# Kernel tuning notes

Measured on AMD Instinct MI355X. Metric: run time of the kernel, lower is better.

The kernel has to match this reference:

```python
import jax, jax.numpy as jnp
import numpy as np
import math

HEAD_DIM = 64
HEAD_NUM = 8  # hidden_dim(512) // head_dim(64)
EPS = 1e-8


def modulated_linear(x, s, weight, aff_w, aff_b):
    # x: [B, N, IN], s: [B, S], weight: [OUT, IN], aff_w: [IN, S], aff_b: [IN]
    style = s @ aff_w.T + aff_b                       # [B, IN]
    w = weight[None, :, :] * style[:, None, :]        # [B, OUT, IN]
    demod = jax.lax.rsqrt(jnp.sum(w * w, axis=2) + EPS)  # [B, OUT]
    w = w * demod[:, :, None]
    return jnp.einsum('bni,boi->bno', x, w)           # [B, N, OUT]


def setup_inputs() -> dict:
    key = jax.random.key(0)
    ks = jax.random.split(key, 8)
    B, N, F, S = 8, 1024, 512, 512
    sc = 1.0 / math.sqrt(F)
    return {
        'x': jax.random.normal(ks[0], (B, N, F), dtype=jnp.float32),
        's': jax.random.normal(ks[1], (B, S), dtype=jnp.float32),
        'k_weight': jax.random.normal(ks[2], (F, F), dtype=jnp.float32) * sc,
        'k_aff_w': jax.random.normal(ks[3], (F, S), dtype=jnp.float32) * sc,
        'k_aff_b': jnp.ones((F,), dtype=jnp.float32),
        'o_weight': jax.random.normal(ks[4], (F, F), dtype=jnp.float32) * sc,
        'o_aff_w': jax.random.normal(ks[5], (F, S), dtype=jnp.float32) * sc,
        'o_aff_b': jnp.ones((F,), dtype=jnp.float32),
    }


def reference(x, s, k_weight, k_aff_w, k_aff_b, o_weight, o_aff_w, o_aff_b):
    B, N, _ = x.shape
    # Original code computes q, k, v all via k_mapping (faithful to the bug).
    kqv = modulated_linear(x, s, k_weight, k_aff_w, k_aff_b)  # [B, N, hidden]
    kqv = kqv.reshape(B, N, HEAD_NUM, HEAD_DIM)               # [B, N, H, D]
    q = k = v = kqv
    scale = 1.0 / math.sqrt(HEAD_DIM)
    scores = jnp.einsum('bnhd,bmhd->bhnm', q, k) * scale      # [B, H, N, N]
    attn = jax.nn.softmax(scores, axis=-1)
    out = jnp.einsum('bhnm,bmhd->bnhd', attn, v)              # [B, N, H, D]
    out = out.reshape(B, N, HEAD_NUM * HEAD_DIM)
    return modulated_linear(out, s, o_weight, o_aff_w, o_aff_b)
```

## Files before the change

### kernel.cpp

```cpp
#include <hip/hip_runtime.h>
#include <stdint.h>

using short8  = __attribute__((ext_vector_type(8))) short;
using f32x4   = __attribute__((ext_vector_type(4))) float;
using float4v = __attribute__((ext_vector_type(4))) float;
using u16x4   = __attribute__((ext_vector_type(4))) unsigned short;

__device__ __forceinline__ unsigned short f2b(float f) {
    union { float f; unsigned int i; } v; v.f = f;
    unsigned int i = v.i;
    unsigned int r = (i + 0x7fffu + ((i >> 16) & 1u)) >> 16;
    return (unsigned short)r;
}
__device__ __forceinline__ short8 ld8(const unsigned short* p) {
    return *reinterpret_cast<const short8*>(p);
}
__device__ __forceinline__ void st8(unsigned short* p, short8 v) {
    *reinterpret_cast<short8*>(p) = v;
}
__device__ __forceinline__ f32x4 mfma16(short8 a, short8 b, f32x4 c) {
    return __builtin_amdgcn_mfma_f32_16x16x32_bf16(a, b, c, 0, 0, 0);
}
__device__ __forceinline__ void stC(float* p, float v)          { *p = v; }
__device__ __forceinline__ void stC(unsigned short* p, float v) { *p = f2b(v); }

__device__ __forceinline__ void gl16(const unsigned short* g, unsigned short* l) {
    __builtin_amdgcn_global_load_lds(
        (const __attribute__((address_space(1))) void*)g,
        (__attribute__((address_space(3))) void*)l,
        16, 0, 0);
}

__device__ __forceinline__ unsigned int cvtpk(float lo, float hi) {
    unsigned int r;
    asm("v_cvt_pk_bf16_f32 %0, %1, %2" : "=v"(r) : "v"(lo), "v"(hi));
    return r;
}
__device__ __forceinline__ void pl32swap(unsigned int& a, unsigned int& b) {
    asm("v_permlane32_swap_b32 %0, %1" : "+v"(a), "+v"(b));
}
__device__ __forceinline__ void pl16swap(unsigned int& a, unsigned int& b) {
    asm("v_permlane16_swap_b32 %0, %1" : "+v"(a), "+v"(b));
}
__device__ __forceinline__ short8 pack4(unsigned int x0, unsigned int x1,
                                        unsigned int x2, unsigned int x3) {
    union { unsigned int u[4]; short8 s; } c;
    c.u[0] = x0; c.u[1] = x1; c.u[2] = x2; c.u[3] = x3;
    return c.s;
}

__global__ __launch_bounds__(256) void cvt_kernel(
    const float* __restrict__ x, unsigned short* __restrict__ xb)
{
    int i = (blockIdx.x * 256 + threadIdx.x) * 8;
    float4v v0 = *reinterpret_cast<const float4v*>(x + i);
    float4v v1 = *reinterpret_cast<const float4v*>(x + i + 4);
    short8 o;
#pragma unroll
    for (int j = 0; j < 4; ++j) o[j] = (short)f2b(v0[j]);
#pragma unroll
    for (int j = 0; j < 4; ++j) o[4 + j] = (short)f2b(v1[j]);
    st8(xb + i, o);
}

__global__ __launch_bounds__(256) void style_kernel(
    const float* __restrict__ s,
    const float* __restrict__ k_aff_w, const float* __restrict__ k_aff_b,
    const float* __restrict__ o_aff_w, const float* __restrict__ o_aff_b,
    float* __restrict__ style)
{
    int wid  = blockIdx.x * 4 + (threadIdx.x >> 6);
    int lane = threadIdx.x & 63;
    int map  = wid >> 12;
    int rem  = wid & 4095;
    int b    = rem >> 9;
    int i    = rem & 511;
    const float* aw = map ? o_aff_w : k_aff_w;
    const float* ab = map ? o_aff_b : k_aff_b;
    const float* sp = s  + b * 512 + lane * 8;
    const float* wp = aw + i * 512 + lane * 8;
    float acc = 0.f;
#pragma unroll
    for (int j = 0; j < 8; ++j) acc += sp[j] * wp[j];
#pragma unroll
    for (int off = 1; off < 64; off <<= 1) acc += __shfl_xor(acc, off, 64);
    if (lane == 0) style[(map * 8 + b) * 512 + i] = acc + ab[i];
}

__global__ __launch_bounds__(256) void modw_kernel(
    const float* __restrict__ k_weight,
    const float* __restrict__ o_weight,
    const float* __restrict__ style,
    unsigned short* __restrict__ wmod)
{
    int wid  = blockIdx.x * 4 + (threadIdx.x >> 6);
    int lane = threadIdx.x & 63;
    int map  = wid >> 12;
    int rem  = wid & 4095;
    int b    = rem >> 9;
    int o    = rem & 511;
    const float* wrow = (map ? o_weight : k_weight) + o * 512 + lane * 8;
    const float* st   = style + (map * 8 + b) * 512 + lane * 8;
    float w[8]; float ss = 0.f;
#pragma unroll
    for (int j = 0; j < 8; ++j) { w[j] = wrow[j] * st[j]; ss += w[j] * w[j]; }
#pragma unroll
    for (int off = 1; off < 64; off <<= 1) ss += __shfl_xor(ss, off, 64);
    float demod = rsqrtf(ss + 1e-8f);
    short8 ov;
#pragma unroll
    for (int j = 0; j < 8; ++j) ov[j] = (short)f2b(w[j] * demod);
    unsigned short* dst = wmod + (((size_t)map * 8 + b) * 512 + o) * 512 + lane * 8;
    *reinterpret_cast<short8*>(dst) = ov;
}

template <typename CT, bool WVT>
__global__ __launch_bounds__(256) void gemm_bt_lds_kernel(
    const unsigned short* __restrict__ A,
    const unsigned short* __restrict__ Bt,
    CT* __restrict__ C,
    unsigned short* __restrict__ VT)
{
    __shared__ __align__(16) unsigned short smem[4 * 4096];

    int blk = blockIdx.x;
    int b   = blk & 7;
    int rem = blk >> 3;
    int mt  = rem & 15;
    int nt  = rem >> 4;
    int tid  = threadIdx.x;
    int w    = tid >> 6;
    int lane = tid & 63;
    int quad = lane >> 4;
    int r    = lane & 15;
    int wm   = w >> 1;
    int wn   = w & 1;

    const unsigned short* Ab = A  + ((size_t)b * 1024 + mt * 64) * 512;
    const unsigned short* Bb = Bt + ((size_t)b * 512  + nt * 64) * 512;

    int lrow = lane >> 3;
    int lunit = (lane & 7) ^ lrow;
    int laneoff = lrow * 512 + lunit * 8;

    f32x4 acc[2][2];
#pragma unroll
    for (int i = 0; i < 2; ++i)
#pragma unroll
        for (int j = 0; j < 2; ++j) acc[i][j] = f32x4{0.f, 0.f, 0.f, 0.f};

    auto stage = [&](int sbuf, int kt) {
        int ko = kt * 64;
        unsigned short* Asb = smem + sbuf * 4096;
        unsigned short* Bsb = smem + 8192 + sbuf * 4096;
#pragma unroll
        for (int c = 0; c < 2; ++c) {
            int chunk = w * 2 + c;
            gl16(Ab + (size_t)chunk * 8 * 512 + laneoff + ko, Asb + chunk * 512);
            gl16(Bb + (size_t)chunk * 8 * 512 + laneoff + ko, Bsb + chunk * 512);
        }
    };
    auto frag = [&](int row, int kh) {
        return row * 64 + ((((kh << 2) | quad) ^ (row & 7)) << 3);
    };

    stage(0, 0);
    __syncthreads();

#pragma unroll
    for (int ks = 0; ks < 8; ++ks) {
        int s = ks & 1;
        if (ks < 7) stage(s ^ 1, ks + 1);
        const unsigned short* Ap = smem + s * 4096;
        const unsigned short* Bp = smem + 8192 + s * 4096;
#pragma unroll
        for (int kh = 0; kh < 2; ++kh) {
            short8 af[2], bf[2];
#pragma unroll
            for (int i = 0; i < 2; ++i)
                af[i] = ld8(Ap + frag(wm * 32 + i * 16 + r, kh));
#pragma unroll
            for (int j = 0; j < 2; ++j)
                bf[j] = ld8(Bp + frag(wn * 32 + j * 16 + r, kh));
#pragma unroll
            for (int i = 0; i < 2; ++i)
#pragma unroll
                for (int j = 0; j < 2; ++j)
                    acc[i][j] = mfma16(af[i], bf[j], acc[i][j]);
        }
        __syncthreads();
    }

    CT* Cb = C + (size_t)b * 1024 * 512;
#pragma unroll
    for (int i = 0; i < 2; ++i)
#pragma unroll
        for (int rr = 0; rr < 4; ++rr) {
            int row = mt * 64 + wm * 32 + i * 16 + quad * 4 + rr;
#pragma unroll
            for (int j = 0; j < 2; ++j) {
                int col = nt * 64 + wn * 32 + j * 16 + r;
                stC(Cb + (size_t)row * 512 + col, acc[i][j][rr]);
            }
        }
    if (WVT) {
        constexpr int TP = 72;
        unsigned short (*Tt)[TP] = reinterpret_cast<unsigned short (*)[TP]>(smem);
#pragma unroll
        for (int i = 0; i < 2; ++i)
#pragma unroll
            for (int j = 0; j < 2; ++j) {
                int d = wn * 32 + j * 16 + r;
#pragma unroll
                for (int rh = 0; rh < 2; ++rh) {
                    int tok = wm * 32 + i * 16 + quad * 4 + rh * 2;
                    unsigned int pv = (unsigned int)f2b(acc[i][j][rh * 2]) |
                                      ((unsigned int)f2b(acc[i][j][rh * 2 + 1]) << 16);
                    *reinterpret_cast<unsigned int*>(&Tt[d][tok]) = pv;
                }
            }
        __syncthreads();
        int d  = tid >> 2;
        int cc = tid & 3;
        const unsigned short* src = &Tt[d][cc * 16];
        unsigned short* dst = VT + ((size_t)(b * 8 + nt) * 64 + d) * 1024 + mt * 64 + cc * 16;
        short8 t0 = ld8(src), t1 = ld8(src + 8);
        st8(dst,     t0);
        st8(dst + 8, t1);
    }
}

__global__ __launch_bounds__(256) void attn_kernel(
    const unsigned short* __restrict__ kqv,
    const unsigned short* __restrict__ vt,
    unsigned short* __restrict__ attn_out)
{
    constexpr int PAD = 72;
    int blk = blockIdx.x;
    int bh = blk & 63;
    int qt = blk >> 6;
    int b  = bh >> 3, h = bh & 7;
    int tid  = threadIdx.x;
    int lane = tid & 63;
    int quad = lane >> 4;
    int r    = lane & 15;

    __shared__ __align__(16) unsigned short klds[2][64][PAD];
    __shared__ __align__(16) unsigned short vlds[2][64][PAD];

    const unsigned short* Mb = kqv + (size_t)b * 1024 * 512;
    int wv = tid >> 6;
    int q0 = qt * 128 + wv * 32;

    const unsigned short* qpA = Mb + (size_t)(q0 + r) * 512 + h * 64 + quad * 8;
    const unsigned short* qpB = Mb + (size_t)(q0 + 16 + r) * 512 + h * 64 + quad * 8;
    short8 aq0 = ld8(qpA), aq1 = ld8(qpA + 32);
    short8 cq0 = ld8(qpB), cq1 = ld8(qpB + 32);

    short8 ones;
#pragma unroll
    for (int j = 0; j < 8; ++j) ones[j] = (short)0x3F80;

    f32x4 z = {0.f, 0.f, 0.f, 0.f};
    f32x4 oA0 = z, oA1 = z, oA2 = z, oA3 = z, lA = z;
    f32x4 oB0 = z, oB1 = z, oB2 = z, oB3 = z, lB = z;

    int srow0 = tid >> 3;
    int srow1 = srow0 + 32;
    int scol  = (tid & 7) * 8;
    const unsigned short* Kg = Mb + h * 64;
    const unsigned short* Vg = vt + (size_t)bh * 64 * 1024;

    {
        short8 k0v = ld8(Kg + (size_t)srow0 * 512 + scol);
        short8 k1v = ld8(Kg + (size_t)srow1 * 512 + scol);
        short8 v0v = ld8(Vg + (size_t)srow0 * 1024 + scol);
        short8 v1v = ld8(Vg + (size_t)srow1 * 1024 + scol);
        st8(&klds[0][srow0][scol], k0v);
        st8(&klds[0][srow1][scol], k1v);
        st8(&vlds[0][srow0][scol], v0v);
        st8(&vlds[0][srow1][scol], v1v);
    }
    __syncthreads();

    const float c  = 0.18033688011112042f;
    const float CM = 28.853900817779268f;

    auto packP = [&](const f32x4* st_, short8& ap0, short8& ap1) {
        unsigned int pk_[4][2];
#pragma unroll
        for (int t = 0; t < 4; ++t)
#pragma unroll
            for (int h2 = 0; h2 < 2; ++h2)
                pk_[t][h2] = cvtpk(exp2f(st_[t][2 * h2]     * c - CM),
                                   exp2f(st_[t][2 * h2 + 1] * c - CM));
        unsigned int a0 = pk_[0][0], b0 = pk_[1][0];
        pl32swap(a0, b0); pl16swap(a0, b0);
        unsigned int a1 = pk_[0][1], b1 = pk_[1][1];
        pl32swap(a1, b1); pl16swap(a1, b1);
        unsigned int c0 = pk_[2][0], d0 = pk_[3][0];
        pl32swap(c0, d0); pl16swap(c0, d0);
        unsigned int c1 = pk_[2][1], d1 = pk_[3][1];
        pl32swap(c1, d1); pl16swap(c1, d1);
        ap0 = pack4(a0, a1, b0, b1);
        ap1 = pack4(c0, c1, d0, d1);
    };

    for (int it = 0; it < 16; ++it) {
        int s = it & 1;
        short8 pk0, pk1, pv0, pv1;
        if (it < 15) {
            int k0n = (it + 1) * 64;
            pk0 = ld8(Kg + (size_t)(k0n + srow0) * 512 + scol);
            pk1 = ld8(Kg + (size_t)(k0n + srow1) * 512 + scol);
            pv0 = ld8(Vg + (size_t)srow0 * 1024 + k0n + scol);
            pv1 = ld8(Vg + (size_t)srow1 * 1024 + k0n + scol);
        }
        f32x4 sA[4], sB[4];
#pragma unroll
        for (int t = 0; t < 4; ++t) {
            short8 ka = ld8(&klds[s][t * 16 + r][quad * 8]);
            short8 kb = ld8(&klds[s][t * 16 + r][32 + quad * 8]);
            f32x4 accA = z, accB = z;
            accA = mfma16(ka, aq0, accA);  accA = mfma16(kb, aq1, accA);
            accB = mfma16(ka, cq0, accB);  accB = mfma16(kb, cq1, accB);
            sA[t] = accA;  sB[t] = accB;
        }
        short8 apA0, apA1, apB0, apB1;
        packP(sA, apA0, apA1);
        packP(sB, apB0, apB1);
        {
            short8 va, vb;
            va = ld8(&vlds[s][0 * 16 + r][quad * 8]);
            vb = ld8(&vlds[s][0 * 16 + r][32 + quad * 8]);
            oA0 = mfma16(apA0, va, oA0);  oA0 = mfma16(apA1, vb, oA0);
            oB0 = mfma16(apB0, va, oB0);  oB0 = mfma16(apB1, vb, oB0);
            va = ld8(&vlds[s][1 * 16 + r][quad * 8]);
            vb = ld8(&vlds[s][1 * 16 + r][32 + quad * 8]);
            oA1 = mfma16(apA0, va, oA1);  oA1 = mfma16(apA1, vb, oA1);
            oB1 = mfma16(apB0, va, oB1);  oB1 = mfma16(apB1, vb, oB1);
            va = ld8(&vlds[s][2 * 16 + r][quad * 8]);
            vb = ld8(&vlds[s][2 * 16 + r][32 + quad * 8]);
            oA2 = mfma16(apA0, va, oA2);  oA2 = mfma16(apA1, vb, oA2);
            oB2 = mfma16(apB0, va, oB2);  oB2 = mfma16(apB1, vb, oB2);
            va = ld8(&vlds[s][3 * 16 + r][quad * 8]);
            vb = ld8(&vlds[s][3 * 16 + r][32 + quad * 8]);
            oA3 = mfma16(apA0, va, oA3);  oA3 = mfma16(apA1, vb, oA3);
            oB3 = mfma16(apB0, va, oB3);  oB3 = mfma16(apB1, vb, oB3);
            lA = mfma16(apA0, ones, lA);  lA = mfma16(apA1, ones, lA);
            lB = mfma16(apB0, ones, lB);  lB = mfma16(apB1, ones, lB);
        }
        if (it < 15) {
            int ns = s ^ 1;
            st8(&klds[ns][srow0][scol], pk0);
            st8(&klds[ns][srow1][scol], pk1);
            st8(&vlds[ns][srow0][scol], pv0);
            st8(&vlds[ns][srow1][scol], pv1);
        }
        __syncthreads();
    }

    unsigned short* ob = attn_out + (size_t)b * 1024 * 512 + (size_t)h * 64;
#pragma unroll
    for (int rr = 0; rr < 4; ++rr) {
        float invA = 1.0f / lA[rr];
        int nA = q0 + quad * 4 + rr;
        unsigned short* orowA = ob + (size_t)nA * 512 + r;
        orowA[0]  = f2b(oA0[rr] * invA);
        orowA[16] = f2b(oA1[rr] * invA);
        orowA[32] = f2b(oA2[rr] * invA);
        orowA[48] = f2b(oA3[rr] * invA);
        float invB = 1.0f / lB[rr];
        int nB = q0 + 16 + quad * 4 + rr;
        unsigned short* orowB = ob + (size_t)nB * 512 + r;
        orowB[0]  = f2b(oB0[rr] * invB);
        orowB[16] = f2b(oB1[rr] * invB);
        orowB[32] = f2b(oB2[rr] * invB);
        orowB[48] = f2b(oB3[rr] * invB);
    }
}

extern "C" void kernel_launch(void* const* d_in, const int* in_sizes, int n_in,
                              void* d_out, int out_size, void* d_ws, size_t ws_size,
                              hipStream_t stream)
{
    const float* x        = (const float*)d_in[0];
    const float* s        = (const float*)d_in[1];
    const float* k_weight = (const float*)d_in[2];
    const float* k_aff_w  = (const float*)d_in[3];
    const float* k_aff_b  = (const float*)d_in[4];
    const float* o_weight = (const float*)d_in[5];
    const float* o_aff_w  = (const float*)d_in[6];
    const float* o_aff_b  = (const float*)d_in[7];
    float* out = (float*)d_out;

    char* ws = (char*)d_ws;
    float* style          = (float*)ws;
    unsigned short* wmod  = (unsigned short*)(ws + 32 * 1024);
    unsigned short* attn  = wmod + (size_t)2 * 8 * 512 * 512;
    unsigned short* kqv   = attn + (size_t)8 * 1024 * 512;
    unsigned short* vt    = kqv  + (size_t)8 * 1024 * 512;
    unsigned short* xb    = vt   + (size_t)64 * 64 * 1024;

    cvt_kernel  <<<2048, 256, 0, stream>>>(x, xb);
    style_kernel<<<2048, 256, 0, stream>>>(s, k_aff_w, k_aff_b, o_aff_w, o_aff_b, style);
    modw_kernel <<<2048, 256, 0, stream>>>(k_weight, o_weight, style, wmod);
    gemm_bt_lds_kernel<unsigned short, true><<<1024, 256, 0, stream>>>(xb, wmod, kqv, vt);
    attn_kernel<<<512, 256, 0, stream>>>(kqv, vt, attn);
    gemm_bt_lds_kernel<float, false><<<1024, 256, 0, stream>>>(attn, wmod + (size_t)8 * 512 * 512, out, nullptr);
}
```

Baseline: 141.1 us.

## Load K and V tiles directly from global memory instead of LDS staging

The attention kernel no longer stages K and V tiles in double-buffered shared memory. Each wave now reads its MFMA operands straight from global memory, relying on L1/L2 caching, and the per-iteration block barriers are gone. The loop is unrolled by two so the compiler can overlap loads. The cost is four waves per block issuing redundant global loads with less coalescing and exposed latency, in exchange for dropping LDS traffic and synchronisation.

```diff
diff --git a/kernel.cpp b/kernel.cpp
--- a/kernel.cpp
+++ b/kernel.cpp
@@ -235,7 +235,6 @@
     const unsigned short* __restrict__ vt,
     unsigned short* __restrict__ attn_out)
 {
-    constexpr int PAD = 72;
     int blk = blockIdx.x;
     int bh = blk & 63;
     int qt = blk >> 6;
@@ -245,9 +244,6 @@
     int quad = lane >> 4;
     int r    = lane & 15;
 
-    __shared__ __align__(16) unsigned short klds[2][64][PAD];
-    __shared__ __align__(16) unsigned short vlds[2][64][PAD];
-
     const unsigned short* Mb = kqv + (size_t)b * 1024 * 512;
     int wv = tid >> 6;
     int q0 = qt * 128 + wv * 32;
@@ -265,23 +261,8 @@
     f32x4 oA0 = z, oA1 = z, oA2 = z, oA3 = z, lA = z;
     f32x4 oB0 = z, oB1 = z, oB2 = z, oB3 = z, lB = z;
 
-    int srow0 = tid >> 3;
-    int srow1 = srow0 + 32;
-    int scol  = (tid & 7) * 8;
     const unsigned short* Kg = Mb + h * 64;
     const unsigned short* Vg = vt + (size_t)bh * 64 * 1024;
-
-    {
-        short8 k0v = ld8(Kg + (size_t)srow0 * 512 + scol);
-        short8 k1v = ld8(Kg + (size_t)srow1 * 512 + scol);
-        short8 v0v = ld8(Vg + (size_t)srow0 * 1024 + scol);
-        short8 v1v = ld8(Vg + (size_t)srow1 * 1024 + scol);
-        st8(&klds[0][srow0][scol], k0v);
-        st8(&klds[0][srow1][scol], k1v);
-        st8(&vlds[0][srow0][scol], v0v);
-        st8(&vlds[0][srow1][scol], v1v);
-    }
-    __syncthreads();
 
     const float c  = 0.18033688011112042f;
     const float CM = 28.853900817779268f;
@@ -306,21 +287,15 @@
         ap1 = pack4(c0, c1, d0, d1);
     };
 
+#pragma unroll 2
     for (int it = 0; it < 16; ++it) {
-        int s = it & 1;
-        short8 pk0, pk1, pv0, pv1;
-        if (it < 15) {
-            int k0n = (it + 1) * 64;
-            pk0 = ld8(Kg + (size_t)(k0n + srow0) * 512 + scol);
-            pk1 = ld8(Kg + (size_t)(k0n + srow1) * 512 + scol);
-            pv0 = ld8(Vg + (size_t)srow0 * 1024 + k0n + scol);
-            pv1 = ld8(Vg + (size_t)srow1 * 1024 + k0n + scol);
-        }
+        int k0 = it * 64;
         f32x4 sA[4], sB[4];
 #pragma unroll
         for (int t = 0; t < 4; ++t) {
-            short8 ka = ld8(&klds[s][t * 16 + r][quad * 8]);
-            short8 kb = ld8(&klds[s][t * 16 + r][32 + quad * 8]);
+            const unsigned short* kp = Kg + (size_t)(k0 + t * 16 + r) * 512 + quad * 8;
+            short8 ka = ld8(kp);
+            short8 kb = ld8(kp + 32);
             f32x4 accA = z, accB = z;
             accA = mfma16(ka, aq0, accA);  accA = mfma16(kb, aq1, accA);
             accB = mfma16(ka, cq0, accB);  accB = mfma16(kb, cq1, accB);
@@ -330,34 +305,26 @@
         packP(sA, apA0, apA1);
         packP(sB, apB0, apB1);
         {
+            const unsigned short* vp0 = Vg + (size_t)(0 * 16 + r) * 1024 + k0 + quad * 8;
+            const unsigned short* vp1 = Vg + (size_t)(1 * 16 + r) * 1024 + k0 + quad * 8;
+            const unsigned short* vp2 = Vg + (size_t)(2 * 16 + r) * 1024 + k0 + quad * 8;
+            const unsigned short* vp3 = Vg + (size_t)(3 * 16 + r) * 1024 + k0 + quad * 8;
             short8 va, vb;
-            va = ld8(&vlds[s][0 * 16 + r][quad * 8]);
-            vb = ld8(&vlds[s][0 * 16 + r][32 + quad * 8]);
+            va = ld8(vp0);  vb = ld8(vp0 + 32);
             oA0 = mfma16(apA0, va, oA0);  oA0 = mfma16(apA1, vb, oA0);
             oB0 = mfma16(apB0, va, oB0);  oB0 = mfma16(apB1, vb, oB0);
-            va = ld8(&vlds[s][1 * 16 + r][quad * 8]);
-            vb = ld8(&vlds[s][1 * 16 + r][32 + quad * 8]);
+            va = ld8(vp1);  vb = ld8(vp1 + 32);
             oA1 = mfma16(apA0, va, oA1);  oA1 = mfma16(apA1, vb, oA1);
             oB1 = mfma16(apB0, va, oB1);  oB1 = mfma16(apB1, vb, oB1);
-            va = ld8(&vlds[s][2 * 16 + r][quad * 8]);
-            vb = ld8(&vlds[s][2 * 16 + r][32 + quad * 8]);
+            va = ld8(vp2);  vb = ld8(vp2 + 32);
             oA2 = mfma16(apA0, va, oA2);  oA2 = mfma16(apA1, vb, oA2);
             oB2 = mfma16(apB0, va, oB2);  oB2 = mfma16(apB1, vb, oB2);
-            va = ld8(&vlds[s][3 * 16 + r][quad * 8]);
-            vb = ld8(&vlds[s][3 * 16 + r][32 + quad * 8]);
+            va = ld8(vp3);  vb = ld8(vp3 + 32);
             oA3 = mfma16(apA0, va, oA3);  oA3 = mfma16(apA1, vb, oA3);
             oB3 = mfma16(apB0, va, oB3);  oB3 = mfma16(apB1, vb, oB3);
             lA = mfma16(apA0, ones, lA);  lA = mfma16(apA1, ones, lA);
             lB = mfma16(apB0, ones, lB);  lB = mfma16(apB1, ones, lB);
         }
-        if (it < 15) {
-            int ns = s ^ 1;
-            st8(&klds[ns][srow0][scol], pk0);
-            st8(&klds[ns][srow1][scol], pk1);
-            st8(&vlds[ns][srow0][scol], pv0);
-            st8(&vlds[ns][srow1][scol], pv1);
-        }
-        __syncthreads();
     }
 
     unsigned short* ob = attn_out + (size_t)b * 1024 * 512 + (size_t)h * 64;
```

Result: slower. 172.5 us (+22.3%).
